# Kernel optimization log

Hardware: AMD Instinct MI355X
Metric: run time of the kernel (lower is better)

Reference implementation:

```python
import jax, jax.numpy as jnp
import numpy as np
from jax import lax

B, T = 8192, 128
HID = 64


def setup_inputs() -> dict:
    key = jax.random.key(0)
    ks = jax.random.split(key, 16)
    actor_ids = jax.random.randint(ks[0], (B, T), 0, 7, dtype=jnp.int32)
    action_ids = jax.random.randint(ks[1], (B, T), 0, 4, dtype=jnp.int32)
    street_ids = jax.random.randint(ks[2], (B, T), 0, 5, dtype=jnp.int32)
    bet_fraction = jax.random.uniform(ks[3], (B, T, 1), dtype=jnp.float32)
    # prefix-valid mask from random lengths (some zero-length rows)
    lengths = jax.random.randint(ks[4], (B,), 0, T + 1)
    valid_mask = jnp.arange(T)[None, :] < lengths[:, None]  # [B,T] bool
    s = 0.1
    params = {
        "E_actor": jax.random.normal(ks[5], (7, 8), jnp.float32) * s,
        "E_action": jax.random.normal(ks[6], (4, 8), jnp.float32) * s,
        "E_street": jax.random.normal(ks[7], (5, 4), jnp.float32) * s,
        "W_proj": jax.random.normal(ks[8], (32, 21), jnp.float32) * s,
        "b_proj": jax.random.normal(ks[9], (32,), jnp.float32) * s,
        "W_ih": jax.random.normal(ks[10], (3 * HID, 32), jnp.float32) * s,
        "W_hh": jax.random.normal(ks[11], (3 * HID, HID), jnp.float32) * s,
        "b_ih": jax.random.normal(ks[12], (3 * HID,), jnp.float32) * s,
        "b_hh": jax.random.normal(ks[13], (3 * HID,), jnp.float32) * s,
    }
    return dict(actor_ids=actor_ids, action_ids=action_ids, street_ids=street_ids,
                bet_fraction=bet_fraction, valid_mask=valid_mask, **params)


def reference(actor_ids, action_ids, street_ids, bet_fraction, valid_mask,
              E_actor, E_action, E_street, W_proj, b_proj,
              W_ih, W_hh, b_ih, b_hh):
    # embed + concat -> [B,T,21]
    feats = jnp.concatenate([E_actor[actor_ids], E_action[action_ids],
                             E_street[street_ids], bet_fraction], axis=-1)
    x = feats @ W_proj.T + b_proj                      # [B,T,32]
    # precompute input-side GRU gates for all timesteps: [B,T,3H]
    xg = x @ W_ih.T + b_ih
    xg_t = jnp.swapaxes(xg, 0, 1)                      # [T,B,3H]
    m_t = jnp.swapaxes(valid_mask, 0, 1)               # [T,B]

    def step(h, inp):
        xg_i, m = inp
        hg = h @ W_hh.T + b_hh                         # [B,3H]
        xr, xz, xn = jnp.split(xg_i, 3, axis=-1)
        hr, hz, hn = jnp.split(hg, 3, axis=-1)
        r = jax.nn.sigmoid(xr + hr)
        z = jax.nn.sigmoid(xz + hz)
        n = jnp.tanh(xn + r * hn)
        h_new = (1.0 - z) * n + z * h
        # only advance hidden state while t < length (prefix-valid mask);
        # final carry equals the GRU hidden at the last valid step, and rows
        # with length 0 stay at the zero init (matches torch masking).
        h = jnp.where(m[:, None], h_new, h)
        return h, None

    h0 = jnp.zeros((x.shape[0], HID), dtype=x.dtype)
    h_final, _ = lax.scan(step, h0, (xg_t, m_t))
    return h_final
```

## Files before the change

kernel.cpp:

```cpp
#include <hip/hip_runtime.h>

#define HID 64
#define TT  128
#define NROWS 8192
#define NGRP (NROWS / 16)
#define LOG2E 1.44269504088896f

typedef _Float16 half8 __attribute__((ext_vector_type(8)));
typedef float    f32x4 __attribute__((ext_vector_type(4)));

__global__ __launch_bounds__(256, 2) void gru_fused(
    const int* __restrict__ actor_ids, const int* __restrict__ action_ids,
    const int* __restrict__ street_ids, const float* __restrict__ bet,
    const int* __restrict__ mask,
    const float* __restrict__ E_actor, const float* __restrict__ E_action,
    const float* __restrict__ E_street, const float* __restrict__ W_proj,
    const float* __restrict__ b_proj, const float* __restrict__ W_ih,
    const float* __restrict__ b_ih, const float* __restrict__ W_hh,
    const float* __restrict__ b_hh, float* __restrict__ out)
{
    __shared__ __align__(16) union {
        float wfs[192][32];
        struct {
            int pb[TT][17];
            __align__(16) _Float16 hb[2][16][72];
            int part[16][16];
            int Lsh[16];
        } c;
    } A;
    __shared__ __align__(16) _Float16 embl[144];
    __shared__ float bfs[192];

    const int tid = threadIdx.x;
    const int wv  = tid >> 6;
    const int l   = tid & 63;
    const int q   = l >> 4;
    const int n   = l & 15;
    const int g   = blockIdx.x;

    for (int i = tid; i < 136; i += 256) {
        int r = i >> 3, m = i & 7;
        float v = 0.f;
        if (r < 7)       v = E_actor[r * 8 + m];
        else if (r < 11) v = E_action[(r - 7) * 8 + m];
        else if (r < 16) v = (m < 4) ? E_street[(r - 11) * 4 + m] : 0.f;
        embl[i] = (_Float16)v;
    }

    if (tid < 192) {
        const int j = tid;
        float wf[21];
        #pragma unroll
        for (int m = 0; m < 21; m++) wf[m] = 0.f;
        float bf = b_ih[j];
        for (int k = 0; k < 32; k++) {
            const float w = W_ih[j * 32 + k];
            bf += w * b_proj[k];
            #pragma unroll
            for (int m = 0; m < 21; m++) wf[m] += w * W_proj[k * 21 + m];
        }
        const float s = (j < 128) ? LOG2E : 2.f * LOG2E;
        #pragma unroll
        for (int m = 0; m < 21; m++) A.wfs[j][m] = wf[m] * s;
        #pragma unroll
        for (int m = 21; m < 32; m++) A.wfs[j][m] = 0.f;
        bfs[j] = bf;
    }
    __syncthreads();

    half8 Af[3], Ah[3][2];
    {
        const int m16 = l & 15, kq = l >> 4;
        #pragma unroll
        for (int g3 = 0; g3 < 3; g3++) {
            const int jr = g3 * 64 + wv * 16 + m16;
            _Float16 v[8];
            #pragma unroll
            for (int m = 0; m < 8; m++) v[m] = (_Float16)A.wfs[jr][kq * 8 + m];
            Af[g3] = *(half8*)v;
            const float s = (g3 < 2) ? LOG2E : 2.f * LOG2E;
            #pragma unroll
            for (int kt = 0; kt < 2; kt++) {
                _Float16 w[8];
                #pragma unroll
                for (int m = 0; m < 8; m++)
                    w[m] = (_Float16)(W_hh[jr * HID + kt * 32 + kq * 8 + m] * s);
                Ah[g3][kt] = *(half8*)w;
            }
        }
    }
    f32x4 biasR, biasZ, biasX, biasH;
    #pragma unroll
    for (int e = 0; e < 4; e++) {
        const int idx = 16 * wv + 4 * q + e;
        biasR[e] = (bfs[idx]      + b_hh[idx])      * LOG2E;
        biasZ[e] = (bfs[64 + idx] + b_hh[64 + idx]) * LOG2E;
        biasX[e] = bfs[128 + idx]  * (2.f * LOG2E);
        biasH[e] = b_hh[128 + idx] * (2.f * LOG2E);
    }
    __syncthreads();

    for (int i = tid; i < 2 * 16 * 72 / 2; i += 256) ((int*)A.c.hb)[i] = 0;
    {
        const int r = tid >> 4, tl = tid & 15;
        const int base = (g * 16 + r) * TT;
        int cnt = 0;
        #pragma unroll
        for (int i = 0; i < 8; i++) {
            const int t = tl + 16 * i;
            const int a = actor_ids[base + t], c = action_ids[base + t];
            const int s = street_ids[base + t];
            const _Float16 f16 = (_Float16)bet[base + t];
            const unsigned fb = (unsigned)*(const unsigned short*)&f16;
            A.c.pb[t][r] = (int)(a | (c << 3) | (s << 5) | (fb << 16));
            cnt += (mask[base + t] != 0);
        }
        A.c.part[r][tl] = cnt;
    }
    __syncthreads();
    if (tid < 16) {
        int L = 0;
        #pragma unroll
        for (int i = 0; i < 16; i++) L += A.c.part[tid][i];
        A.c.Lsh[tid] = L;
    }
    __syncthreads();

    const int Ln = A.c.Lsh[n];
    int Lmax = Ln;
    #pragma unroll
    for (int k = 1; k < 16; k <<= 1) {
        const int o = __shfl_xor(Lmax, k);
        Lmax = (o > Lmax) ? o : Lmax;
    }

    const bool isq2 = (q == 2);
    const int sh = (q == 1) ? 3 : (q == 2) ? 5 : 0;
    const int mk = (q == 1) ? 3 : (q == 3) ? 0 : 7;
    const int of = (q == 1) ? 7 : (q == 2) ? 11 : (q == 3) ? 16 : 0;

    float h[4] = {0.f, 0.f, 0.f, 0.f};

    f32x4 xR, xZ, xX;
    {
        const int p = A.c.pb[0][n];
        const int eidx = ((p >> sh) & mk) + of;
        half8 Bf = *(const half8*)&embl[eidx * 8];
        uint4* bu = (uint4*)&Bf;
        bu->z = isq2 ? ((unsigned)p >> 16) : bu->z;
        xR = __builtin_amdgcn_mfma_f32_16x16x32_f16(Af[0], Bf, biasR, 0, 0, 0);
        xZ = __builtin_amdgcn_mfma_f32_16x16x32_f16(Af[1], Bf, biasZ, 0, 0, 0);
        xX = __builtin_amdgcn_mfma_f32_16x16x32_f16(Af[2], Bf, biasX, 0, 0, 0);
    }

    for (int t = 0; t < Lmax; t++) {
        const int buf = t & 1;
        const half8 Bh0 = *(const half8*)&A.c.hb[buf][n][q * 8];
        const half8 Bh1 = *(const half8*)&A.c.hb[buf][n][32 + q * 8];
        f32x4 aR = __builtin_amdgcn_mfma_f32_16x16x32_f16(Ah[0][0], Bh0, xR, 0, 0, 0);
        aR = __builtin_amdgcn_mfma_f32_16x16x32_f16(Ah[0][1], Bh1, aR, 0, 0, 0);
        f32x4 aZ = __builtin_amdgcn_mfma_f32_16x16x32_f16(Ah[1][0], Bh0, xZ, 0, 0, 0);
        aZ = __builtin_amdgcn_mfma_f32_16x16x32_f16(Ah[1][1], Bh1, aZ, 0, 0, 0);
        f32x4 aH = __builtin_amdgcn_mfma_f32_16x16x32_f16(Ah[2][0], Bh0, biasH, 0, 0, 0);
        aH = __builtin_amdgcn_mfma_f32_16x16x32_f16(Ah[2][1], Bh1, aH, 0, 0, 0);
        const f32x4 aXc = xX;

        {
            const int tn = (t + 1 < TT) ? t + 1 : TT - 1;
            const int p = A.c.pb[tn][n];
            const int eidx = ((p >> sh) & mk) + of;
            half8 Bf = *(const half8*)&embl[eidx * 8];
            uint4* bu = (uint4*)&Bf;
            bu->z = isq2 ? ((unsigned)p >> 16) : bu->z;
            xR = __builtin_amdgcn_mfma_f32_16x16x32_f16(Af[0], Bf, biasR, 0, 0, 0);
            xZ = __builtin_amdgcn_mfma_f32_16x16x32_f16(Af[1], Bf, biasZ, 0, 0, 0);
            xX = __builtin_amdgcn_mfma_f32_16x16x32_f16(Af[2], Bf, biasX, 0, 0, 0);
        }

        const bool live = (t < Ln);
        _Float16 hp[4];
        #pragma unroll
        for (int e = 0; e < 4; e++) {
            const float r = __builtin_amdgcn_rcpf(1.f + __builtin_amdgcn_exp2f(-aR[e]));
            const float z = __builtin_amdgcn_rcpf(1.f + __builtin_amdgcn_exp2f(-aZ[e]));
            const float y2 = aXc[e] + r * aH[e];
            const float nn = 1.f - 2.f * __builtin_amdgcn_rcpf(1.f + __builtin_amdgcn_exp2f(y2));
            const float hv = nn + z * (h[e] - nn);
            h[e] = live ? hv : h[e];
            hp[e] = (_Float16)h[e];
        }
        *(uint2*)&A.c.hb[buf ^ 1][n][16 * wv + 4 * q] = *(uint2*)hp;
        __syncthreads();
    }

    float4 o = make_float4(h[0], h[1], h[2], h[3]);
    *(float4*)&out[(g * 16 + n) * HID + 16 * wv + 4 * q] = o;
}

extern "C" void kernel_launch(void* const* d_in, const int* in_sizes, int n_in,
                              void* d_out, int out_size, void* d_ws, size_t ws_size,
                              hipStream_t stream) {
    const int*   actor_ids  = (const int*)d_in[0];
    const int*   action_ids = (const int*)d_in[1];
    const int*   street_ids = (const int*)d_in[2];
    const float* bet        = (const float*)d_in[3];
    const int*   vmask      = (const int*)d_in[4];
    const float* E_actor    = (const float*)d_in[5];
    const float* E_action   = (const float*)d_in[6];
    const float* E_street   = (const float*)d_in[7];
    const float* W_proj     = (const float*)d_in[8];
    const float* b_proj     = (const float*)d_in[9];
    const float* W_ih       = (const float*)d_in[10];
    const float* W_hh       = (const float*)d_in[11];
    const float* b_ih       = (const float*)d_in[12];
    const float* b_hh       = (const float*)d_in[13];
    float*       out        = (float*)d_out;

    gru_fused<<<NGRP, 256, 0, stream>>>(actor_ids, action_ids, street_ids, bet,
                                        vmask, E_actor, E_action, E_street,
                                        W_proj, b_proj, W_ih, b_ih, W_hh, b_hh,
                                        out);
}
```

Baseline: 166.0 us.

## Process two 16-row groups per block to interleave independent GRU recurrences

```diff
diff --git a/kernel.cpp b/kernel.cpp
--- a/kernel.cpp
+++ b/kernel.cpp
@@ -3,13 +3,13 @@
 #define HID 64
 #define TT  128
 #define NROWS 8192
-#define NGRP (NROWS / 16)
+#define NBLK 256
 #define LOG2E 1.44269504088896f
 
 typedef _Float16 half8 __attribute__((ext_vector_type(8)));
 typedef float    f32x4 __attribute__((ext_vector_type(4)));
 
-__global__ __launch_bounds__(256, 2) void gru_fused(
+__global__ __launch_bounds__(256) void gru_fused(
     const int* __restrict__ actor_ids, const int* __restrict__ action_ids,
     const int* __restrict__ street_ids, const float* __restrict__ bet,
     const int* __restrict__ mask,
@@ -22,10 +22,10 @@
     __shared__ __align__(16) union {
         float wfs[192][32];
         struct {
-            int pb[TT][17];
-            __align__(16) _Float16 hb[2][16][72];
-            int part[16][16];
-            int Lsh[16];
+            int pb[2][TT][17];
+            __align__(16) _Float16 hb[2][2][16][72];
+            int part[32][8];
+            int Lsh[32];
         } c;
     } A;
     __shared__ __align__(16) _Float16 embl[144];
@@ -100,34 +100,36 @@
     }
     __syncthreads();
 
-    for (int i = tid; i < 2 * 16 * 72 / 2; i += 256) ((int*)A.c.hb)[i] = 0;
-    {
-        const int r = tid >> 4, tl = tid & 15;
-        const int base = (g * 16 + r) * TT;
+    for (int i = tid; i < (int)(sizeof(A.c.hb) / 4); i += 256) ((int*)A.c.hb)[i] = 0;
+    {
+        const int r = tid >> 3, tl = tid & 7;
+        const int s = r >> 4, rr = r & 15;
+        const int base = (g * 32 + r) * TT;
         int cnt = 0;
         #pragma unroll
-        for (int i = 0; i < 8; i++) {
-            const int t = tl + 16 * i;
+        for (int i = 0; i < 16; i++) {
+            const int t = tl + 8 * i;
             const int a = actor_ids[base + t], c = action_ids[base + t];
-            const int s = street_ids[base + t];
+            const int st = street_ids[base + t];
             const _Float16 f16 = (_Float16)bet[base + t];
             const unsigned fb = (unsigned)*(const unsigned short*)&f16;
-            A.c.pb[t][r] = (int)(a | (c << 3) | (s << 5) | (fb << 16));
+            A.c.pb[s][t][rr] = (int)(a | (c << 3) | (st << 5) | (fb << 16));
             cnt += (mask[base + t] != 0);
         }
         A.c.part[r][tl] = cnt;
     }
     __syncthreads();
-    if (tid < 16) {
+    if (tid < 32) {
         int L = 0;
         #pragma unroll
-        for (int i = 0; i < 16; i++) L += A.c.part[tid][i];
+        for (int i = 0; i < 8; i++) L += A.c.part[tid][i];
         A.c.Lsh[tid] = L;
     }
     __syncthreads();
 
-    const int Ln = A.c.Lsh[n];
-    int Lmax = Ln;
+    const int Ln0 = A.c.Lsh[n];
+    const int Ln1 = A.c.Lsh[16 + n];
+    int Lmax = (Ln0 > Ln1) ? Ln0 : Ln1;
     #pragma unroll
     for (int k = 1; k < 16; k <<= 1) {
         const int o = __shfl_xor(Lmax, k);
@@ -139,62 +141,103 @@
     const int mk = (q == 1) ? 3 : (q == 3) ? 0 : 7;
     const int of = (q == 1) ? 7 : (q == 2) ? 11 : (q == 3) ? 16 : 0;
 
-    float h[4] = {0.f, 0.f, 0.f, 0.f};
-
-    f32x4 xR, xZ, xX;
-    {
-        const int p = A.c.pb[0][n];
+    float h0[4] = {0.f, 0.f, 0.f, 0.f};
+    float h1[4] = {0.f, 0.f, 0.f, 0.f};
+
+    f32x4 xR0, xZ0, xX0, xR1, xZ1, xX1;
+    #pragma unroll
+    for (int s = 0; s < 2; s++) {
+        const int p = A.c.pb[s][0][n];
         const int eidx = ((p >> sh) & mk) + of;
         half8 Bf = *(const half8*)&embl[eidx * 8];
         uint4* bu = (uint4*)&Bf;
         bu->z = isq2 ? ((unsigned)p >> 16) : bu->z;
-        xR = __builtin_amdgcn_mfma_f32_16x16x32_f16(Af[0], Bf, biasR, 0, 0, 0);
-        xZ = __builtin_amdgcn_mfma_f32_16x16x32_f16(Af[1], Bf, biasZ, 0, 0, 0);
-        xX = __builtin_amdgcn_mfma_f32_16x16x32_f16(Af[2], Bf, biasX, 0, 0, 0);
+        f32x4 r_ = __builtin_amdgcn_mfma_f32_16x16x32_f16(Af[0], Bf, biasR, 0, 0, 0);
+        f32x4 z_ = __builtin_amdgcn_mfma_f32_16x16x32_f16(Af[1], Bf, biasZ, 0, 0, 0);
+        f32x4 x_ = __builtin_amdgcn_mfma_f32_16x16x32_f16(Af[2], Bf, biasX, 0, 0, 0);
+        if (s == 0) { xR0 = r_; xZ0 = z_; xX0 = x_; }
+        else        { xR1 = r_; xZ1 = z_; xX1 = x_; }
     }
 
     for (int t = 0; t < Lmax; t++) {
         const int buf = t & 1;
-        const half8 Bh0 = *(const half8*)&A.c.hb[buf][n][q * 8];
-        const half8 Bh1 = *(const half8*)&A.c.hb[buf][n][32 + q * 8];
-        f32x4 aR = __builtin_amdgcn_mfma_f32_16x16x32_f16(Ah[0][0], Bh0, xR, 0, 0, 0);
-        aR = __builtin_amdgcn_mfma_f32_16x16x32_f16(Ah[0][1], Bh1, aR, 0, 0, 0);
-        f32x4 aZ = __builtin_amdgcn_mfma_f32_16x16x32_f16(Ah[1][0], Bh0, xZ, 0, 0, 0);
-        aZ = __builtin_amdgcn_mfma_f32_16x16x32_f16(Ah[1][1], Bh1, aZ, 0, 0, 0);
-        f32x4 aH = __builtin_amdgcn_mfma_f32_16x16x32_f16(Ah[2][0], Bh0, biasH, 0, 0, 0);
-        aH = __builtin_amdgcn_mfma_f32_16x16x32_f16(Ah[2][1], Bh1, aH, 0, 0, 0);
-        const f32x4 aXc = xX;
-
+        const half8 B00 = *(const half8*)&A.c.hb[0][buf][n][q * 8];
+        const half8 B01 = *(const half8*)&A.c.hb[0][buf][n][32 + q * 8];
+        const half8 B10 = *(const half8*)&A.c.hb[1][buf][n][q * 8];
+        const half8 B11 = *(const half8*)&A.c.hb[1][buf][n][32 + q * 8];
+
+        f32x4 aR0 = __builtin_amdgcn_mfma_f32_16x16x32_f16(Ah[0][0], B00, xR0, 0, 0, 0);
+        f32x4 aR1 = __builtin_amdgcn_mfma_f32_16x16x32_f16(Ah[0][0], B10, xR1, 0, 0, 0);
+        f32x4 aZ0 = __builtin_amdgcn_mfma_f32_16x16x32_f16(Ah[1][0], B00, xZ0, 0, 0, 0);
+        f32x4 aZ1 = __builtin_amdgcn_mfma_f32_16x16x32_f16(Ah[1][0], B10, xZ1, 0, 0, 0);
+        f32x4 aH0 = __builtin_amdgcn_mfma_f32_16x16x32_f16(Ah[2][0], B00, biasH, 0, 0, 0);
+        f32x4 aH1 = __builtin_amdgcn_mfma_f32_16x16x32_f16(Ah[2][0], B10, biasH, 0, 0, 0);
+        aR0 = __builtin_amdgcn_mfma_f32_16x16x32_f16(Ah[0][1], B01, aR0, 0, 0, 0);
+        aR1 = __builtin_amdgcn_mfma_f32_16x16x32_f16(Ah[0][1], B11, aR1, 0, 0, 0);
+        aZ0 = __builtin_amdgcn_mfma_f32_16x16x32_f16(Ah[1][1], B01, aZ0, 0, 0, 0);
+        aZ1 = __builtin_amdgcn_mfma_f32_16x16x32_f16(Ah[1][1], B11, aZ1, 0, 0, 0);
+        aH0 = __builtin_amdgcn_mfma_f32_16x16x32_f16(Ah[2][1], B01, aH0, 0, 0, 0);
+        aH1 = __builtin_amdgcn_mfma_f32_16x16x32_f16(Ah[2][1], B11, aH1, 0, 0, 0);
+        const f32x4 aX0 = xX0, aX1 = xX1;
+
+        const int tn = (t + 1 < TT) ? t + 1 : TT - 1;
         {
-            const int tn = (t + 1 < TT) ? t + 1 : TT - 1;
-            const int p = A.c.pb[tn][n];
+            const int p = A.c.pb[0][tn][n];
             const int eidx = ((p >> sh) & mk) + of;
             half8 Bf = *(const half8*)&embl[eidx * 8];
             uint4* bu = (uint4*)&Bf;
             bu->z = isq2 ? ((unsigned)p >> 16) : bu->z;
-            xR = __builtin_amdgcn_mfma_f32_16x16x32_f16(Af[0], Bf, biasR, 0, 0, 0);
-            xZ = __builtin_amdgcn_mfma_f32_16x16x32_f16(Af[1], Bf, biasZ, 0, 0, 0);
-            xX = __builtin_amdgcn_mfma_f32_16x16x32_f16(Af[2], Bf, biasX, 0, 0, 0);
-        }
-
-        const bool live = (t < Ln);
-        _Float16 hp[4];
+            xR0 = __builtin_amdgcn_mfma_f32_16x16x32_f16(Af[0], Bf, biasR, 0, 0, 0);
+            xZ0 = __builtin_amdgcn_mfma_f32_16x16x32_f16(Af[1], Bf, biasZ, 0, 0, 0);
+            xX0 = __builtin_amdgcn_mfma_f32_16x16x32_f16(Af[2], Bf, biasX, 0, 0, 0);
+        }
+        {
+            const int p = A.c.pb[1][tn][n];
+            const int eidx = ((p >> sh) & mk) + of;
+            half8 Bf = *(const half8*)&embl[eidx * 8];
+            uint4* bu = (uint4*)&Bf;
+            bu->z = isq2 ? ((unsigned)p >> 16) : bu->z;
+            xR1 = __builtin_amdgcn_mfma_f32_16x16x32_f16(Af[0], Bf, biasR, 0, 0, 0);
+            xZ1 = __builtin_amdgcn_mfma_f32_16x16x32_f16(Af[1], Bf, biasZ, 0, 0, 0);
+            xX1 = __builtin_amdgcn_mfma_f32_16x16x32_f16(Af[2], Bf, biasX, 0, 0, 0);
+        }
+
+        const bool lv0 = (t < Ln0), lv1 = (t < Ln1);
+        _Float16 hp0[4], hp1[4];
         #pragma unroll
         for (int e = 0; e < 4; e++) {
-            const float r = __builtin_amdgcn_rcpf(1.f + __builtin_amdgcn_exp2f(-aR[e]));
-            const float z = __builtin_amdgcn_rcpf(1.f + __builtin_amdgcn_exp2f(-aZ[e]));
-            const float y2 = aXc[e] + r * aH[e];
-            const float nn = 1.f - 2.f * __builtin_amdgcn_rcpf(1.f + __builtin_amdgcn_exp2f(y2));
-            const float hv = nn + z * (h[e] - nn);
-            h[e] = live ? hv : h[e];
-            hp[e] = (_Float16)h[e];
-        }
-        *(uint2*)&A.c.hb[buf ^ 1][n][16 * wv + 4 * q] = *(uint2*)hp;
+            {
+                const float r = __builtin_amdgcn_rcpf(1.f + __builtin_amdgcn_exp2f(-aR0[e]));
+                const float z = __builtin_amdgcn_rcpf(1.f + __builtin_amdgcn_exp2f(-aZ0[e]));
+                const float y2 = aX0[e] + r * aH0[e];
+                const float nn = 1.f - 2.f * __builtin_amdgcn_rcpf(1.f + __builtin_amdgcn_exp2f(y2));
+                const float hv = nn + z * (h0[e] - nn);
+                h0[e] = lv0 ? hv : h0[e];
+                hp0[e] = (_Float16)h0[e];
+            }
+            {
+                const float r = __builtin_amdgcn_rcpf(1.f + __builtin_amdgcn_exp2f(-aR1[e]));
+                const float z = __builtin_amdgcn_rcpf(1.f + __builtin_amdgcn_exp2f(-aZ1[e]));
+                const float y2 = aX1[e] + r * aH1[e];
+                const float nn = 1.f - 2.f * __builtin_amdgcn_rcpf(1.f + __builtin_amdgcn_exp2f(y2));
+                const float hv = nn + z * (h1[e] - nn);
+                h1[e] = lv1 ? hv : h1[e];
+                hp1[e] = (_Float16)h1[e];
+            }
+        }
+        *(uint2*)&A.c.hb[0][buf ^ 1][n][16 * wv + 4 * q] = *(uint2*)hp0;
+        *(uint2*)&A.c.hb[1][buf ^ 1][n][16 * wv + 4 * q] = *(uint2*)hp1;
         __syncthreads();
     }
 
-    float4 o = make_float4(h[0], h[1], h[2], h[3]);
-    *(float4*)&out[(g * 16 + n) * HID + 16 * wv + 4 * q] = o;
+    {
+        float4 o = make_float4(h0[0], h0[1], h0[2], h0[3]);
+        *(float4*)&out[(g * 32 + n) * HID + 16 * wv + 4 * q] = o;
+    }
+    {
+        float4 o = make_float4(h1[0], h1[1], h1[2], h1[3]);
+        *(float4*)&out[(g * 32 + 16 + n) * HID + 16 * wv + 4 * q] = o;
+    }
 }
 
 extern "C" void kernel_launch(void* const* d_in, const int* in_sizes, int n_in,
@@ -216,7 +259,7 @@
     const float* b_hh       = (const float*)d_in[13];
     float*       out        = (float*)d_out;
 
-    gru_fused<<<NGRP, 256, 0, stream>>>(actor_ids, action_ids, street_ids, bet,
+    gru_fused<<<NBLK, 256, 0, stream>>>(actor_ids, action_ids, street_ids, bet,
                                         vmask, E_actor, E_action, E_street,
                                         W_proj, b_proj, W_ih, b_ih, W_hh, b_hh,
                                         out);
```

Result: slower. 195.6 us (+17.9%).

## Sort rows by sequence length so each 16-row group runs to similar length

Applied to the files above, without the earlier changes.

```diff
diff --git a/kernel.cpp b/kernel.cpp
--- a/kernel.cpp
+++ b/kernel.cpp
@@ -9,34 +9,66 @@
 typedef _Float16 half8 __attribute__((ext_vector_type(8)));
 typedef float    f32x4 __attribute__((ext_vector_type(4)));
 
+__global__ __launch_bounds__(256) void lens(const int* __restrict__ mask,
+                                            int* __restrict__ Lrow)
+{
+    __shared__ int part[16][16];
+    const int j = threadIdx.x;
+    const int r = j >> 4, tl = j & 15;
+    for (int it = 0; it < 8; it++) {
+        const int row = blockIdx.x * 128 + it * 16 + r;
+        const int base = row * TT;
+        int cnt = 0;
+        #pragma unroll
+        for (int i = 0; i < 8; i++) cnt += (mask[base + tl + 16 * i] != 0);
+        part[r][tl] = cnt;
+        __syncthreads();
+        if (j < 16) {
+            int L = 0;
+            #pragma unroll
+            for (int i = 0; i < 16; i++) L += part[j][i];
+            Lrow[blockIdx.x * 128 + it * 16 + j] = L;
+        }
+        __syncthreads();
+    }
+}
+
 __global__ __launch_bounds__(256, 2) void gru_fused(
     const int* __restrict__ actor_ids, const int* __restrict__ action_ids,
     const int* __restrict__ street_ids, const float* __restrict__ bet,
-    const int* __restrict__ mask,
     const float* __restrict__ E_actor, const float* __restrict__ E_action,
     const float* __restrict__ E_street, const float* __restrict__ W_proj,
     const float* __restrict__ b_proj, const float* __restrict__ W_ih,
     const float* __restrict__ b_ih, const float* __restrict__ W_hh,
-    const float* __restrict__ b_hh, float* __restrict__ out)
+    const float* __restrict__ b_hh, const int* __restrict__ Lrow,
+    float* __restrict__ out)
 {
     __shared__ __align__(16) union {
+        struct {
+            int hist[129];
+            int pref[129];
+            int cand[512];
+            int ncand;
+        } s;
         float wfs[192][32];
         struct {
             int pb[TT][17];
             __align__(16) _Float16 hb[2][16][72];
-            int part[16][16];
-            int Lsh[16];
         } c;
     } A;
     __shared__ __align__(16) _Float16 embl[144];
     __shared__ float bfs[192];
+    __shared__ int ordr[16], Lw[16];
 
     const int tid = threadIdx.x;
     const int wv  = tid >> 6;
     const int l   = tid & 63;
     const int q   = l >> 4;
     const int n   = l & 15;
-    const int g   = blockIdx.x;
+
+    const int b  = blockIdx.x;
+    const int g  = (b & 1) ? (NGRP - 1 - (b >> 1)) : (b >> 1);
+    const int w0 = g * 16;
 
     for (int i = tid; i < 136; i += 256) {
         int r = i >> 3, m = i & 7;
@@ -47,6 +79,50 @@
         embl[i] = (_Float16)v;
     }
 
+    int Lreg[32];
+    #pragma unroll
+    for (int i = 0; i < 32; i++) Lreg[i] = Lrow[i * 256 + tid];
+    for (int i = tid; i < 129; i += 256) A.s.hist[i] = 0;
+    if (tid == 0) A.s.ncand = 0;
+    if (tid < 16) { ordr[tid] = 0; Lw[tid] = 0; }
+    __syncthreads();
+    #pragma unroll
+    for (int i = 0; i < 32; i++) atomicAdd(&A.s.hist[Lreg[i]], 1);
+    __syncthreads();
+    if (tid < 129) A.s.pref[tid] = A.s.hist[tid];
+    __syncthreads();
+    for (int d = 1; d < 129; d <<= 1) {
+        int v = 0;
+        if (tid < 129 && tid >= d) v = A.s.pref[tid - d];
+        __syncthreads();
+        if (tid < 129) A.s.pref[tid] += v;
+        __syncthreads();
+    }
+    #pragma unroll
+    for (int i = 0; i < 32; i++) {
+        const int L = Lreg[i];
+        const int e = A.s.pref[L] - A.s.hist[L];
+        if (e < w0 + 16 && A.s.pref[L] > w0) {
+            const int k = atomicAdd(&A.s.ncand, 1);
+            if (k < 512) A.s.cand[k] = (L << 13) | (i * 256 + tid);
+        }
+    }
+    __syncthreads();
+    {
+        const int nc = (A.s.ncand < 512) ? A.s.ncand : 512;
+        for (int i = tid; i < nc; i += 256) {
+            const int key = A.s.cand[i];
+            const int L = key >> 13, lo = L << 13;
+            int r = A.s.pref[L] - A.s.hist[L];
+            for (int jj = 0; jj < nc; jj++) {
+                const int k2 = A.s.cand[jj];
+                r += (k2 >= lo && k2 < key);
+            }
+            if (r >= w0 && r < w0 + 16) { ordr[r - w0] = key & 8191; Lw[r - w0] = L; }
+        }
+    }
+    __syncthreads();
+
     if (tid < 192) {
         const int j = tid;
         float wf[21];
@@ -103,8 +179,7 @@
     for (int i = tid; i < 2 * 16 * 72 / 2; i += 256) ((int*)A.c.hb)[i] = 0;
     {
         const int r = tid >> 4, tl = tid & 15;
-        const int base = (g * 16 + r) * TT;
-        int cnt = 0;
+        const int base = ordr[r] * TT;
         #pragma unroll
         for (int i = 0; i < 8; i++) {
             const int t = tl + 16 * i;
@@ -113,33 +188,19 @@
             const _Float16 f16 = (_Float16)bet[base + t];
             const unsigned fb = (unsigned)*(const unsigned short*)&f16;
             A.c.pb[t][r] = (int)(a | (c << 3) | (s << 5) | (fb << 16));
-            cnt += (mask[base + t] != 0);
-        }
-        A.c.part[r][tl] = cnt;
-    }
-    __syncthreads();
-    if (tid < 16) {
-        int L = 0;
-        #pragma unroll
-        for (int i = 0; i < 16; i++) L += A.c.part[tid][i];
-        A.c.Lsh[tid] = L;
-    }
-    __syncthreads();
-
-    const int Ln = A.c.Lsh[n];
-    int Lmax = Ln;
-    #pragma unroll
-    for (int k = 1; k < 16; k <<= 1) {
-        const int o = __shfl_xor(Lmax, k);
-        Lmax = (o > Lmax) ? o : Lmax;
-    }
-
+        }
+    }
+
+    const int myrow = ordr[n];
+    const int Ln    = Lw[n];
+    const int Lmax  = Lw[15];
     const bool isq2 = (q == 2);
     const int sh = (q == 1) ? 3 : (q == 2) ? 5 : 0;
     const int mk = (q == 1) ? 3 : (q == 3) ? 0 : 7;
     const int of = (q == 1) ? 7 : (q == 2) ? 11 : (q == 3) ? 16 : 0;
 
     float h[4] = {0.f, 0.f, 0.f, 0.f};
+    __syncthreads();
 
     f32x4 xR, xZ, xX;
     {
@@ -194,7 +255,7 @@
     }
 
     float4 o = make_float4(h[0], h[1], h[2], h[3]);
-    *(float4*)&out[(g * 16 + n) * HID + 16 * wv + 4 * q] = o;
+    *(float4*)&out[myrow * HID + 16 * wv + 4 * q] = o;
 }
 
 extern "C" void kernel_launch(void* const* d_in, const int* in_sizes, int n_in,
@@ -215,9 +276,11 @@
     const float* b_ih       = (const float*)d_in[12];
     const float* b_hh       = (const float*)d_in[13];
     float*       out        = (float*)d_out;
-
+    int*         Lrow       = (int*)d_ws;
+
+    lens<<<64, 256, 0, stream>>>(vmask, Lrow);
     gru_fused<<<NGRP, 256, 0, stream>>>(actor_ids, action_ids, street_ids, bet,
-                                        vmask, E_actor, E_action, E_street,
-                                        W_proj, b_proj, W_ih, b_ih, W_hh, b_hh,
+                                        E_actor, E_action, E_street, W_proj,
+                                        b_proj, W_ih, b_ih, W_hh, b_hh, Lrow,
                                         out);
 }
```

Result: slower. 172.6 us (+4.0%).
